# Performance work log

Measured on AMD Instinct MI355X. Metric: run time of the kernel, lower is better.

Reference implementation:

```python
import jax, jax.numpy as jnp
import numpy as np

H = 8      # head_nums
D = 64     # head_planes
SCALE = D ** -0.5


def setup_inputs() -> dict:
    key = jax.random.key(0)
    ks = jax.random.split(key, 7)
    B, Nq, Nkv = 2, 2048, 2048
    Cq, Ck, I = 1024, 768, H * D
    return {
        "x": jax.random.normal(ks[0], (B, Nq, Cq), jnp.float32),
        "context": jax.random.normal(ks[1], (B, Nkv, Ck), jnp.float32),
        "Wq": jax.random.normal(ks[2], (Cq, I), jnp.float32) * (Cq ** -0.5),
        "Wk": jax.random.normal(ks[3], (Ck, I), jnp.float32) * (Ck ** -0.5),
        "Wv": jax.random.normal(ks[4], (Ck, I), jnp.float32) * (Ck ** -0.5),
        "Wo": jax.random.normal(ks[5], (I, Cq), jnp.float32) * (I ** -0.5),
        "bo": jnp.zeros((Cq,), jnp.float32),
    }


def reference(x, context, Wq, Wk, Wv, Wo, bo):
    B, Nq, _ = x.shape
    Nkv = context.shape[1]
    # projections (bias-free, as in to_q/to_k/to_v)
    q = (x @ Wq).reshape(B, Nq, H, D)        # b i h d
    k = (context @ Wk).reshape(B, Nkv, H, D)  # b j h d
    v = (context @ Wv).reshape(B, Nkv, H, D)
    # scaled dot-product attention, full [B,H,Nq,Nkv] scores as in original
    sim = jnp.einsum('bihd,bjhd->bhij', q, k) * SCALE
    attn = jax.nn.softmax(sim, axis=-1)
    out = jnp.einsum('bhij,bjhd->bihd', attn, v).reshape(B, Nq, H * D)
    # to_out linear (dropout_prob=0.0 -> identity)
    return out @ Wo + bo
```

## Files before the change

### kernel.cpp

```cpp
#include <hip/hip_runtime.h>
#include <hip/hip_bf16.h>

typedef __hip_bfloat16 bf16;
typedef __attribute__((ext_vector_type(8))) short short8;
typedef __attribute__((ext_vector_type(4))) float f32x4;
typedef __attribute__((ext_vector_type(16))) float f32x16;

#define MFMA16(a, b, c) __builtin_amdgcn_mfma_f32_16x16x32_bf16((a), (b), (c), 0, 0, 0)
#define MFMA32(a, b, c) __builtin_amdgcn_mfma_f32_32x32x16_bf16((a), (b), (c), 0, 0, 0)

#define BATCH 2
#define NQ 2048
#define NKV 2048
#define HEADS 8
#define DHEAD 64
#define CQ 1024
#define CK 768
#define IDIM 512
#define SCALE 0.125f

__device__ __forceinline__ short8 ld8(const bf16* p) {
    return *(const short8*)p;
}

__device__ __forceinline__ void async_ld16(const bf16* g, bf16* l) {
    __builtin_amdgcn_global_load_lds((__attribute__((address_space(1))) const void*)g,
                                     (__attribute__((address_space(3))) void*)l,
                                     16, 0, 0);
}

__global__ __launch_bounds__(256) void prologue(
    const float* __restrict__ x, const float* __restrict__ ctx,
    const float* __restrict__ Wq, const float* __restrict__ Wk,
    const float* __restrict__ Wv, const float* __restrict__ Wo,
    bf16* __restrict__ Xb, bf16* __restrict__ Cb,
    bf16* __restrict__ WqT, bf16* __restrict__ WkT,
    bf16* __restrict__ WvT, bf16* __restrict__ WoT) {
    __shared__ float tile[64][65];
    const int t = threadIdx.x;
    const int bx = blockIdx.x;

    if (bx < 3584) {
        int idx = bx * 256 + t;
        const int NX8 = (4096 * 1024) / 8;
        const float4* srcp;
        bf16* dstp;
        if (idx < NX8) {
            srcp = (const float4*)x + (size_t)idx * 2;
            dstp = Xb + (size_t)idx * 8;
        } else {
            int j = idx - NX8;
            srcp = (const float4*)ctx + (size_t)j * 2;
            dstp = Cb + (size_t)j * 8;
        }
        float4 v0 = srcp[0], v1 = srcp[1];
        bf16 tmp[8] = {__float2bfloat16(v0.x), __float2bfloat16(v0.y),
                       __float2bfloat16(v0.z), __float2bfloat16(v0.w),
                       __float2bfloat16(v1.x), __float2bfloat16(v1.y),
                       __float2bfloat16(v1.z), __float2bfloat16(v1.w)};
        *(short8*)dstp = *(short8*)tmp;
        return;
    }

    int tb = bx - 3584;
    const float* src; bf16* dst; int R, C, ti;
    if (tb < 128)      { src = Wq; dst = WqT; R = 1024; C = 512;  ti = tb; }
    else if (tb < 224) { src = Wk; dst = WkT; R = 768;  C = 512;  ti = tb - 128; }
    else if (tb < 320) { src = Wv; dst = WvT; R = 768;  C = 512;  ti = tb - 224; }
    else               { src = Wo; dst = WoT; R = 512;  C = 1024; ti = tb - 320; }
    const int tilesC = C >> 6;
    const int tr = ti / tilesC, tc = ti - tr * tilesC;

    {
        int row = t >> 4;
        int c4 = (t & 15) * 4;
#pragma unroll
        for (int p = 0; p < 4; ++p) {
            float4 v = *(const float4*)&src[(size_t)(tr * 64 + p * 16 + row) * C + tc * 64 + c4];
            tile[p * 16 + row][c4 + 0] = v.x;
            tile[p * 16 + row][c4 + 1] = v.y;
            tile[p * 16 + row][c4 + 2] = v.z;
            tile[p * 16 + row][c4 + 3] = v.w;
        }
    }
    __syncthreads();
    {
        int oc = t >> 2;
        int r0 = (t & 3) * 16;
        bf16 tmp[16];
#pragma unroll
        for (int j = 0; j < 16; ++j)
            tmp[j] = __float2bfloat16(tile[r0 + j][oc]);
        bf16* dp = dst + (size_t)(tc * 64 + oc) * R + tr * 64 + r0;
        *(short8*)dp = *(short8*)&tmp[0];
        *(short8*)(dp + 8) = *(short8*)&tmp[8];
    }
}

__global__ __launch_bounds__(256) void qkv_gemm(
    const bf16* __restrict__ Xb, const bf16* __restrict__ Cb,
    const bf16* __restrict__ WqT, const bf16* __restrict__ WkT,
    const bf16* __restrict__ WvT,
    bf16* __restrict__ Qb, bf16* __restrict__ Kb, bf16* __restrict__ Vt) {
    __shared__ bf16 At[2][64 * 64];
    __shared__ bf16 Bts[2][128 * 64];

    const int z = blockIdx.z;
    const bf16* A  = (z == 0) ? Xb : Cb;
    const bf16* Bt = (z == 0) ? WqT : (z == 1) ? WkT : WvT;
    const int K = (z == 0) ? 1024 : 768;

    const int t = threadIdx.x;
    const int wave = t >> 6;
    const int lane = t & 63;
    const int n15 = lane & 15;
    const int quad = lane >> 4;
    const int wm = wave >> 1;
    const int wn = wave & 1;
    const int bm = blockIdx.y;
    const int bn = blockIdx.x;

    f32x4 acc[2][4] = {};

    const bf16* Ablk = A + (size_t)bm * 64 * K;
    const bf16* Bblk = Bt + (size_t)bn * 128 * K;

    int ar[2], ac[2], br[4], bc[4];
#pragma unroll
    for (int i = 0; i < 2; ++i) {
        int g = i * 256 + t;
        ar[i] = g >> 3; ac[i] = ((g & 7) ^ (ar[i] & 7)) * 8;
    }
#pragma unroll
    for (int i = 0; i < 4; ++i) {
        int g = i * 256 + t;
        br[i] = g >> 3; bc[i] = ((g & 7) ^ (br[i] & 7)) * 8;
    }

#pragma unroll
    for (int i = 0; i < 2; ++i)
        async_ld16(Ablk + ar[i] * K + ac[i], &At[0][(i * 256 + t) * 8]);
#pragma unroll
    for (int i = 0; i < 4; ++i)
        async_ld16(Bblk + br[i] * K + bc[i], &Bts[0][(i * 256 + t) * 8]);
    __syncthreads();

    for (int k0 = 0; k0 < K; k0 += 64) {
        const int p = (k0 >> 6) & 1;
        if (k0 + 64 < K) {
            const int q = p ^ 1;
            const int kn = k0 + 64;
#pragma unroll
            for (int i = 0; i < 2; ++i)
                async_ld16(Ablk + ar[i] * K + kn + ac[i], &At[q][(i * 256 + t) * 8]);
#pragma unroll
            for (int i = 0; i < 4; ++i)
                async_ld16(Bblk + br[i] * K + kn + bc[i], &Bts[q][(i * 256 + t) * 8]);
        }

#pragma unroll
        for (int kh = 0; kh < 2; ++kh) {
            short8 af[2], bfr[4];
#pragma unroll
            for (int mt = 0; mt < 2; ++mt) {
                int R = wm * 32 + mt * 16 + n15;
                af[mt] = ld8(&At[p][R * 64 + (((kh * 4 + quad) ^ (R & 7)) * 8)]);
            }
#pragma unroll
            for (int nt = 0; nt < 4; ++nt) {
                int R = wn * 64 + nt * 16 + n15;
                bfr[nt] = ld8(&Bts[p][R * 64 + (((kh * 4 + quad) ^ (R & 7)) * 8)]);
            }
#pragma unroll
            for (int mt = 0; mt < 2; ++mt)
#pragma unroll
                for (int nt = 0; nt < 4; ++nt)
                    acc[mt][nt] = MFMA16(af[mt], bfr[nt], acc[mt][nt]);
        }

        __syncthreads();
    }

    bf16* C = (z == 0) ? Qb : (z == 1) ? Kb : Vt;
#pragma unroll
    for (int mt = 0; mt < 2; ++mt) {
#pragma unroll
        for (int nt = 0; nt < 4; ++nt) {
            int col = bn * 128 + wn * 64 + nt * 16 + n15;
#pragma unroll
            for (int r = 0; r < 4; ++r) {
                int row = bm * 64 + wm * 32 + mt * 16 + quad * 4 + r;
                bf16 v = __float2bfloat16(acc[mt][nt][r]);
                if (z < 2) {
                    C[(size_t)row * 512 + col] = v;
                } else {
                    int b = row >> 11, j = row & 2047;
                    int h = col >> 6, d = col & 63;
                    C[(size_t)(((b << 3) + h) * 64 + d) * 2048 + j] = v;
                }
            }
        }
    }
}

__global__ __launch_bounds__(256) void out_gemm(const bf16* __restrict__ A,
                                                const bf16* __restrict__ Bt,
                                                const float* __restrict__ bias,
                                                float* __restrict__ C) {
    const int K = 512, N = 1024;
    __shared__ bf16 At[2][64 * 64];
    __shared__ bf16 Bts[2][128 * 64];

    const int t = threadIdx.x;
    const int wave = t >> 6;
    const int lane = t & 63;
    const int n15 = lane & 15;
    const int quad = lane >> 4;
    const int wm = wave >> 1;
    const int wn = wave & 1;
    const int bm = blockIdx.y;
    const int bn = blockIdx.x;

    f32x4 acc[2][4] = {};

    const bf16* Ablk = A + (size_t)bm * 64 * K;
    const bf16* Bblk = Bt + (size_t)bn * 128 * K;

    int ar[2], ac[2], br[4], bc[4];
#pragma unroll
    for (int i = 0; i < 2; ++i) {
        int g = i * 256 + t;
        ar[i] = g >> 3; ac[i] = ((g & 7) ^ (ar[i] & 7)) * 8;
    }
#pragma unroll
    for (int i = 0; i < 4; ++i) {
        int g = i * 256 + t;
        br[i] = g >> 3; bc[i] = ((g & 7) ^ (br[i] & 7)) * 8;
    }

#pragma unroll
    for (int i = 0; i < 2; ++i)
        async_ld16(Ablk + ar[i] * K + ac[i], &At[0][(i * 256 + t) * 8]);
#pragma unroll
    for (int i = 0; i < 4; ++i)
        async_ld16(Bblk + br[i] * K + bc[i], &Bts[0][(i * 256 + t) * 8]);
    __syncthreads();

    for (int k0 = 0; k0 < K; k0 += 64) {
        const int p = (k0 >> 6) & 1;
        if (k0 + 64 < K) {
            const int q = p ^ 1;
            const int kn = k0 + 64;
#pragma unroll
            for (int i = 0; i < 2; ++i)
                async_ld16(Ablk + ar[i] * K + kn + ac[i], &At[q][(i * 256 + t) * 8]);
#pragma unroll
            for (int i = 0; i < 4; ++i)
                async_ld16(Bblk + br[i] * K + kn + bc[i], &Bts[q][(i * 256 + t) * 8]);
        }

#pragma unroll
        for (int kh = 0; kh < 2; ++kh) {
            short8 af[2], bfr[4];
#pragma unroll
            for (int mt = 0; mt < 2; ++mt) {
                int R = wm * 32 + mt * 16 + n15;
                af[mt] = ld8(&At[p][R * 64 + (((kh * 4 + quad) ^ (R & 7)) * 8)]);
            }
#pragma unroll
            for (int nt = 0; nt < 4; ++nt) {
                int R = wn * 64 + nt * 16 + n15;
                bfr[nt] = ld8(&Bts[p][R * 64 + (((kh * 4 + quad) ^ (R & 7)) * 8)]);
            }
#pragma unroll
            for (int mt = 0; mt < 2; ++mt)
#pragma unroll
                for (int nt = 0; nt < 4; ++nt)
                    acc[mt][nt] = MFMA16(af[mt], bfr[nt], acc[mt][nt]);
        }

        __syncthreads();
    }

#pragma unroll
    for (int mt = 0; mt < 2; ++mt) {
#pragma unroll
        for (int nt = 0; nt < 4; ++nt) {
            int col = bn * 128 + wn * 64 + nt * 16 + n15;
            float bv = bias[col];
#pragma unroll
            for (int r = 0; r < 4; ++r) {
                int row = bm * 64 + wm * 32 + mt * 16 + quad * 4 + r;
                C[(size_t)row * N + col] = acc[mt][nt][r] + bv;
            }
        }
    }
}

__global__ __launch_bounds__(512, 1) void flash_attn(const bf16* __restrict__ Q,
                                                     const bf16* __restrict__ K,
                                                     const bf16* __restrict__ Vt,
                                                     bf16* __restrict__ O) {
    __shared__ bf16 Kt[2][2][64 * 64];
    __shared__ bf16 Vte[2][2][64 * 64];
    __shared__ bf16 Pa[8][32 * 72];
    __shared__ float Lc[4][32];

    const int t = threadIdx.x;
    const int wave = t >> 6;
    const int g = wave >> 1;
    const int kh = wave & 1;
    const int lane = t & 63;
    const int n31 = lane & 31;
    const int half = lane >> 5;

    const int L = blockIdx.x;
    const int bh = L & 15;
    const int b = bh >> 3, h = bh & 7;
    const int q0 = (L >> 4) * 128;
    const int qw = q0 + g * 32;

    const bf16* Qp = Q + ((size_t)(b * NQ + qw) * IDIM + h * DHEAD);
    const bf16* Kp = K + ((size_t)b * NKV * IDIM + h * DHEAD)
                       + (size_t)(kh * 1024) * IDIM;
    const bf16* Vp = Vt + (size_t)((b * HEADS + h) * DHEAD) * NKV + kh * 1024;
    bf16* Pw = Pa[wave];

    short8 qa[4];
#pragma unroll
    for (int ks = 0; ks < 4; ++ks)
        qa[ks] = ld8(Qp + n31 * IDIM + ks * 16 + half * 8);

    const int u = g * 64 + lane;
    const int s0 = u, s1 = u + 256;
    const int r0 = s0 >> 3, c0 = (s0 & 7) ^ (r0 & 7);
    const int r1 = s1 >> 3, c1 = (s1 & 7) ^ (r1 & 7);
    const bf16* kg0 = Kp + r0 * IDIM + c0 * 8;
    const bf16* kg1 = Kp + r1 * IDIM + c1 * 8;
    const bf16* vg0 = Vp + (size_t)r0 * NKV + c0 * 8;
    const bf16* vg1 = Vp + (size_t)r1 * NKV + c1 * 8;

    f32x16 o[2] = {};
    float lsum = 0.f;

    async_ld16(kg0, &Kt[0][kh][s0 * 8]);
    async_ld16(kg1, &Kt[0][kh][s1 * 8]);
    async_ld16(vg0, &Vte[0][kh][s0 * 8]);
    async_ld16(vg1, &Vte[0][kh][s1 * 8]);
    __syncthreads();

    for (int key0 = 0; key0 < 1024; key0 += 64) {
        const int p = (key0 >> 6) & 1;
        if (key0 + 64 < 1024) {
            const int q = p ^ 1;
            const int kn = key0 + 64;
            async_ld16(kg0 + (size_t)kn * IDIM, &Kt[q][kh][s0 * 8]);
            async_ld16(kg1 + (size_t)kn * IDIM, &Kt[q][kh][s1 * 8]);
            async_ld16(vg0 + kn, &Vte[q][kh][s0 * 8]);
            async_ld16(vg1 + kn, &Vte[q][kh][s1 * 8]);
        }

        f32x16 s[2] = {};
#pragma unroll
        for (int su = 0; su < 2; ++su) {
            const int row = su * 32 + n31;
            const bf16* kr = &Kt[p][kh][row * 64];
            const int rs = row & 7;
#pragma unroll
            for (int ks = 0; ks < 4; ++ks) {
                short8 ka = ld8(kr + (((ks * 2 + half) ^ rs) * 8));
                s[su] = MFMA32(ka, qa[ks], s[su]);
            }
        }

#pragma unroll
        for (int su = 0; su < 2; ++su) {
#pragma unroll
            for (int rg = 0; rg < 4; ++rg) {
                float p0 = __expf(s[su][rg * 4 + 0] * SCALE);
                float p1 = __expf(s[su][rg * 4 + 1] * SCALE);
                float p2 = __expf(s[su][rg * 4 + 2] * SCALE);
                float p3 = __expf(s[su][rg * 4 + 3] * SCALE);
                lsum += (p0 + p1) + (p2 + p3);
                bf16 pk[4] = {__float2bfloat16(p0), __float2bfloat16(p1),
                              __float2bfloat16(p2), __float2bfloat16(p3)};
                *(uint2*)&Pw[n31 * 72 + su * 32 + rg * 8 + half * 4] = *(uint2*)pk;
            }
        }
        asm volatile("s_waitcnt lgkmcnt(0)" ::: "memory");

        short8 pb[4];
#pragma unroll
        for (int ks2 = 0; ks2 < 4; ++ks2)
            pb[ks2] = ld8(&Pw[n31 * 72 + ks2 * 16 + half * 8]);

#pragma unroll
        for (int dt = 0; dt < 2; ++dt) {
            const int row = dt * 32 + n31;
            const bf16* vr = &Vte[p][kh][row * 64];
            const int rs = row & 7;
#pragma unroll
            for (int ks2 = 0; ks2 < 4; ++ks2) {
                short8 va = ld8(vr + (((ks2 * 2 + half) ^ rs) * 8));
                o[dt] = MFMA32(va, pb[ks2], o[dt]);
            }
        }
        __syncthreads();
    }

    lsum += __shfl_xor(lsum, 32, 64);

    float* Comb = (float*)&Kt[0][0][0];
    if (kh == 1) {
#pragma unroll
        for (int dt = 0; dt < 2; ++dt)
#pragma unroll
            for (int r = 0; r < 16; ++r) {
                int d = dt * 32 + (r & 3) + 8 * (r >> 2) + 4 * half;
                Comb[((g * 64 + d) << 5) + n31] = o[dt][r];
            }
        if (lane < 32) Lc[g][lane] = lsum;
    }
    __syncthreads();
    if (kh == 0) {
        float inv = 1.0f / (lsum + Lc[g][n31]);
#pragma unroll
        for (int dt = 0; dt < 2; ++dt) {
#pragma unroll
            for (int rg = 0; rg < 4; ++rg) {
                int db = dt * 32 + rg * 8 + half * 4;
                bf16 pk[4];
#pragma unroll
                for (int i = 0; i < 4; ++i) {
                    float v = o[dt][rg * 4 + i] + Comb[((g * 64 + db + i) << 5) + n31];
                    pk[i] = __float2bfloat16(v * inv);
                }
                *(uint2*)&Pa[g * 2][n31 * 72 + db] = *(uint2*)pk;
            }
        }
    }
    __syncthreads();

    {
        int ql = t >> 2, seg = t & 3;
        const bf16* src = &Pa[(ql >> 5) * 2][(ql & 31) * 72 + seg * 16];
        short8 a0 = ld8(src);
        short8 a1 = ld8(src + 8);
        bf16* dst = O + ((size_t)(b * NQ + q0 + ql) * IDIM + h * DHEAD + seg * 16);
        *(short8*)dst = a0;
        *(short8*)(dst + 8) = a1;
    }
}

extern "C" void kernel_launch(void* const* d_in, const int* in_sizes, int n_in,
                              void* d_out, int out_size, void* d_ws, size_t ws_size,
                              hipStream_t stream) {
    (void)in_sizes; (void)n_in; (void)out_size; (void)ws_size;

    const float* x   = (const float*)d_in[0];
    const float* ctx = (const float*)d_in[1];
    const float* Wq  = (const float*)d_in[2];
    const float* Wk  = (const float*)d_in[3];
    const float* Wv  = (const float*)d_in[4];
    const float* Wo  = (const float*)d_in[5];
    const float* bo  = (const float*)d_in[6];
    float* out = (float*)d_out;

    char* ws = (char*)d_ws;
    bf16* Xb  = (bf16*)(ws + 0);
    bf16* Cb  = (bf16*)(ws + 8388608);
    bf16* WqT = (bf16*)(ws + 14680064);
    bf16* WkT = (bf16*)(ws + 15728640);
    bf16* WvT = (bf16*)(ws + 16515072);
    bf16* WoT = (bf16*)(ws + 17301504);
    bf16* Qb  = (bf16*)(ws + 18350080);
    bf16* Kb  = (bf16*)(ws + 22544384);
    bf16* Vt  = (bf16*)(ws + 26738688);
    bf16* Ob  = (bf16*)(ws + 30932992);

    prologue<<<4032, 256, 0, stream>>>(x, ctx, Wq, Wk, Wv, Wo,
                                       Xb, Cb, WqT, WkT, WvT, WoT);

    qkv_gemm<<<dim3(4, 64, 3), 256, 0, stream>>>(Xb, Cb, WqT, WkT, WvT, Qb, Kb, Vt);

    flash_attn<<<256, 512, 0, stream>>>(Qb, Kb, Vt, Ob);

    out_gemm<<<dim3(8, 64), 256, 0, stream>>>(Ob, WoT, bo, out);
}
```

Measured before the change: 152.5 us.

## Drop K/V double buffering in flash attention to cut LDS and raise occupancy

Replaces the double-buffered K/V shared-memory tiles with single buffers. Each iteration now loads its tile and synchronizes before computing, instead of prefetching the next tile. The launch bound is raised from 1 to 4 blocks per CU, and the cross-wave output combine scratch is remapped onto the smaller K/V buffers. The aim is more resident blocks per CU from the lower LDS footprint. The cost is losing load/compute overlap and tighter register limits that could cause spills. With only 256 blocks, the extra occupancy may not be usable.

```diff
diff --git a/kernel.cpp b/kernel.cpp
--- a/kernel.cpp
+++ b/kernel.cpp
@@ -297,12 +297,12 @@
     }
 }
 
-__global__ __launch_bounds__(512, 1) void flash_attn(const bf16* __restrict__ Q,
+__global__ __launch_bounds__(512, 4) void flash_attn(const bf16* __restrict__ Q,
                                                      const bf16* __restrict__ K,
                                                      const bf16* __restrict__ Vt,
                                                      bf16* __restrict__ O) {
-    __shared__ bf16 Kt[2][2][64 * 64];
-    __shared__ bf16 Vte[2][2][64 * 64];
+    __shared__ bf16 Kt[2][64 * 64];
+    __shared__ bf16 Vte[2][64 * 64];
     __shared__ bf16 Pa[8][32 * 72];
     __shared__ float Lc[4][32];
 
@@ -339,32 +339,26 @@
     const bf16* kg1 = Kp + r1 * IDIM + c1 * 8;
     const bf16* vg0 = Vp + (size_t)r0 * NKV + c0 * 8;
     const bf16* vg1 = Vp + (size_t)r1 * NKV + c1 * 8;
+    bf16* kl0 = &Kt[kh][s0 * 8];
+    bf16* kl1 = &Kt[kh][s1 * 8];
+    bf16* vl0 = &Vte[kh][s0 * 8];
+    bf16* vl1 = &Vte[kh][s1 * 8];
 
     f32x16 o[2] = {};
     float lsum = 0.f;
 
-    async_ld16(kg0, &Kt[0][kh][s0 * 8]);
-    async_ld16(kg1, &Kt[0][kh][s1 * 8]);
-    async_ld16(vg0, &Vte[0][kh][s0 * 8]);
-    async_ld16(vg1, &Vte[0][kh][s1 * 8]);
-    __syncthreads();
-
     for (int key0 = 0; key0 < 1024; key0 += 64) {
-        const int p = (key0 >> 6) & 1;
-        if (key0 + 64 < 1024) {
-            const int q = p ^ 1;
-            const int kn = key0 + 64;
-            async_ld16(kg0 + (size_t)kn * IDIM, &Kt[q][kh][s0 * 8]);
-            async_ld16(kg1 + (size_t)kn * IDIM, &Kt[q][kh][s1 * 8]);
-            async_ld16(vg0 + kn, &Vte[q][kh][s0 * 8]);
-            async_ld16(vg1 + kn, &Vte[q][kh][s1 * 8]);
-        }
+        async_ld16(kg0 + (size_t)key0 * IDIM, kl0);
+        async_ld16(kg1 + (size_t)key0 * IDIM, kl1);
+        async_ld16(vg0 + key0, vl0);
+        async_ld16(vg1 + key0, vl1);
+        __syncthreads();
 
         f32x16 s[2] = {};
 #pragma unroll
         for (int su = 0; su < 2; ++su) {
             const int row = su * 32 + n31;
-            const bf16* kr = &Kt[p][kh][row * 64];
+            const bf16* kr = &Kt[kh][row * 64];
             const int rs = row & 7;
 #pragma unroll
             for (int ks = 0; ks < 4; ++ks) {
@@ -397,7 +391,7 @@
 #pragma unroll
         for (int dt = 0; dt < 2; ++dt) {
             const int row = dt * 32 + n31;
-            const bf16* vr = &Vte[p][kh][row * 64];
+            const bf16* vr = &Vte[kh][row * 64];
             const int rs = row & 7;
 #pragma unroll
             for (int ks2 = 0; ks2 < 4; ++ks2) {
@@ -410,14 +404,14 @@
 
     lsum += __shfl_xor(lsum, 32, 64);
 
-    float* Comb = (float*)&Kt[0][0][0];
+    float* Cg = ((g & 2) ? (float*)&Vte[0][0] : (float*)&Kt[0][0]) + (g & 1) * (64 * 32);
     if (kh == 1) {
 #pragma unroll
         for (int dt = 0; dt < 2; ++dt)
 #pragma unroll
             for (int r = 0; r < 16; ++r) {
                 int d = dt * 32 + (r & 3) + 8 * (r >> 2) + 4 * half;
-                Comb[((g * 64 + d) << 5) + n31] = o[dt][r];
+                Cg[(d << 5) + n31] = o[dt][r];
             }
         if (lane < 32) Lc[g][lane] = lsum;
     }
@@ -432,7 +426,7 @@
                 bf16 pk[4];
 #pragma unroll
                 for (int i = 0; i < 4; ++i) {
-                    float v = o[dt][rg * 4 + i] + Comb[((g * 64 + db + i) << 5) + n31];
+                    float v = o[dt][rg * 4 + i] + Cg[((db + i) << 5) + n31];
                     pk[i] = __float2bfloat16(v * inv);
                 }
                 *(uint2*)&Pa[g * 2][n31 * 72 + db] = *(uint2*)pk;
```

New measurement: 156.4 us. 2.6% more time.
